# Kernel tuning notes

Measured on AMD Instinct MI355X. Metric: run time of the kernel, lower is better.

The kernel has to match this reference:

```python
import jax, jax.numpy as jnp
import numpy as np

B, S, D, H = 64, 512, 256, 512  # batch, seq_len, input embed dim, LSTM hidden dim


def setup_inputs() -> dict:
    key = jax.random.key(0)
    k1, k2, k3, k4, k5 = jax.random.split(key, 5)
    scale = 1.0 / np.sqrt(H)
    return {
        "state_embeds": jax.random.normal(k1, (B, S, D), dtype=jnp.float32),
        "W_ih": jax.random.normal(k2, (4 * H, D), dtype=jnp.float32) * scale,
        "W_hh": jax.random.normal(k3, (4 * H, H), dtype=jnp.float32) * scale,
        "b_ih": jax.random.normal(k4, (4 * H,), dtype=jnp.float32) * scale,
        "b_hh": jax.random.normal(k5, (4 * H,), dtype=jnp.float32) * scale,
        "h0": jnp.zeros((B, H), dtype=jnp.float32),
        "c0": jnp.zeros((B, H), dtype=jnp.float32),
    }


def reference(state_embeds, W_ih, W_hh, b_ih, b_hh, h0, c0):
    # Precompute the input projection for all timesteps at once: [B, S, 4H]
    x_proj = jnp.einsum("bsd,gd->bsg", state_embeds, W_ih) + b_ih + b_hh

    def step(carry, xt):
        h, c = carry
        gates = xt + h @ W_hh.T  # [B, 4H]
        i, f, g, o = jnp.split(gates, 4, axis=-1)
        i = jax.nn.sigmoid(i)
        f = jax.nn.sigmoid(f)
        g = jnp.tanh(g)
        o = jax.nn.sigmoid(o)
        c_new = f * c + i * g
        h_new = o * jnp.tanh(c_new)
        return (h_new, c_new), h_new

    (hT, cT), hs = jax.lax.scan(step, (h0, c0), jnp.swapaxes(x_proj, 0, 1))
    embeddings = jnp.swapaxes(hs, 0, 1)  # [B, S, H]
    # hidden state is detached in the original; here we just return it
    return embeddings, hT, cT
```

## Files before the change

kernel.cpp:

```cpp
#include <hip/hip_runtime.h>
#include <hip/hip_bf16.h>


#define NB 64
#define NS 512
#define ND 256
#define NH 512
#define FLAG_MAGIC 0x41000000
#define PLANE_ELEMS (NB * NH)

typedef __bf16 bf16x8 __attribute__((ext_vector_type(8)));
typedef float  f32x4  __attribute__((ext_vector_type(4)));

union Frag {
  bf16x8 v;
  unsigned long long u[2];
  __bf16 e[8];
};

__device__ __forceinline__ float bf2f(__bf16 b) {
  unsigned short us = __builtin_bit_cast(unsigned short, b);
  unsigned int ui = ((unsigned int)us) << 16;
  return __builtin_bit_cast(float, ui);
}

__device__ __forceinline__ void hilo8(const float* vals, Frag& fh, Frag& fl) {
#pragma unroll
  for (int j = 0; j < 8; ++j) {
    __bf16 hi = (__bf16)vals[j];
    float r = vals[j] - bf2f(hi);
    fh.e[j] = hi;
    fl.e[j] = (__bf16)r;
  }
}

__device__ __forceinline__ float fsigmoid(float x) {
  return 1.0f / (1.0f + __expf(-x));
}
__device__ __forceinline__ float ftanh(float x) {
  float t = fminf(fmaxf(2.0f * x, -30.0f), 30.0f);
  float e = __expf(t);
  return (e - 1.0f) / (e + 1.0f);
}

__global__ __launch_bounds__(128, 1)
void lstm_xp(const float* __restrict__ x,
             const float* __restrict__ Wih,
             const float* __restrict__ Whh,
             const float* __restrict__ bih,
             const float* __restrict__ bhh,
             const float* __restrict__ h0,
             const float* __restrict__ c0,
             float* __restrict__ out,
             int* __restrict__ flags,
             unsigned short* __restrict__ hring,
             unsigned short* __restrict__ lring,
             float4* __restrict__ xproj)
{
  const int tid  = threadIdx.x;
  const int lane = tid & 63;
  const int wv   = tid >> 6;
  const int team = blockIdx.x >> 6;
  const int wg   = blockIdx.x & 63;
  const int l15  = lane & 15;
  const int quad = lane >> 4;
  const int hb   = wg * 8 + wv * 4;
  const int myb  = team * 16 + l15;
  const int myh  = hb + quad;

  int* flagsT = flags + team * 64;
  if (tid == 0)
    __hip_atomic_store(flagsT + wg, FLAG_MAGIC, __ATOMIC_RELAXED,
                       __HIP_MEMORY_SCOPE_AGENT);

  const int jA = l15 >> 2;
  const int gA = l15 & 3;
  const int rA = gA * NH + hb + jA;
  bf16x8 Ahi[24], Alo[24];
  {
    const float* wi = Wih + rA * ND;
    const float* wh = Whh + rA * NH;
#pragma unroll
    for (int c = 0; c < 24; ++c) {
      int k0 = c * 32 + quad * 8;
      const float* src = (c < 8) ? (wi + k0) : (wh + (k0 - 256));
      float4 f0 = *(const float4*)(src);
      float4 f1 = *(const float4*)(src + 4);
      float vals[8] = {f0.x, f0.y, f0.z, f0.w, f1.x, f1.y, f1.z, f1.w};
      Frag fh, fl;
      hilo8(vals, fh, fl);
      Ahi[c] = fh.v;
      Alo[c] = fl.v;
    }
  }

  float bias[4];
#pragma unroll
  for (int g = 0; g < 4; ++g)
    bias[g] = bih[g * NH + myh] + bhh[g * NH + myh];

  float4* xpw = xproj + ((size_t)(blockIdx.x * 2 + wv)) * NS * 64;
#pragma unroll 1
  for (int t = 0; t < NS; ++t) {
    float4 xf[16];
    const float* xr = x + (myb * NS + t) * ND + quad * 8;
#pragma unroll
    for (int c = 0; c < 8; ++c) {
      xf[2 * c]     = *(const float4*)(xr + 32 * c);
      xf[2 * c + 1] = *(const float4*)(xr + 32 * c + 4);
    }
    f32x4 a_hh = {bias[0], bias[1], bias[2], bias[3]};
    f32x4 a_hl = {0.f, 0.f, 0.f, 0.f};
    f32x4 a_lh = {0.f, 0.f, 0.f, 0.f};
#pragma unroll
    for (int c = 0; c < 8; ++c) {
      float vals[8] = {xf[2*c].x, xf[2*c].y, xf[2*c].z, xf[2*c].w,
                       xf[2*c+1].x, xf[2*c+1].y, xf[2*c+1].z, xf[2*c+1].w};
      Frag bh, bl;
      hilo8(vals, bh, bl);
      a_hh = __builtin_amdgcn_mfma_f32_16x16x32_bf16(Ahi[c], bh.v, a_hh, 0, 0, 0);
      a_hl = __builtin_amdgcn_mfma_f32_16x16x32_bf16(Ahi[c], bl.v, a_hl, 0, 0, 0);
      a_lh = __builtin_amdgcn_mfma_f32_16x16x32_bf16(Alo[c], bh.v, a_lh, 0, 0, 0);
    }
    float4 xpv;
    xpv.x = a_hh[0] + a_hl[0] + a_lh[0];
    xpv.y = a_hh[1] + a_hl[1] + a_lh[1];
    xpv.z = a_hh[2] + a_hl[2] + a_lh[2];
    xpv.w = a_hh[3] + a_hl[3] + a_lh[3];
    xpw[t * 64 + lane] = xpv;
  }
  asm volatile("s_waitcnt vmcnt(0)" ::: "memory");

  float c_st  = c0[myb * NH + myh];
  float h_val = 0.0f;
  float4 xp_cur = xpw[lane];

#pragma unroll 1
  for (int t = 0; t < NS; ++t) {
    f32x4 a_hh = {0.f, 0.f, 0.f, 0.f};
    f32x4 a_hl = {0.f, 0.f, 0.f, 0.f};
    f32x4 a_lh = {0.f, 0.f, 0.f, 0.f};

    if (t > 0) {
      while (true) {
        int fl = __hip_atomic_load(flagsT + lane, __ATOMIC_RELAXED,
                                   __HIP_MEMORY_SCOPE_AGENT);
        unsigned int d = (unsigned int)(fl - FLAG_MAGIC);
        if (__all(d >= (unsigned int)t && d <= 512u)) break;
        __builtin_amdgcn_s_sleep(1);
      }
      asm volatile("" ::: "memory");

      const unsigned short* hbp = hring + (t - 1) * PLANE_ELEMS + myb * NH + quad * 8;
      const unsigned short* lbp = lring + (t - 1) * PLANE_ELEMS + myb * NH + quad * 8;
#pragma unroll
      for (int c = 8; c < 24; ++c) {
        int off = 32 * (c - 8);
        Frag bh, bl;
        bh.v = *(const bf16x8*)(hbp + off);
        bl.v = *(const bf16x8*)(lbp + off);
        a_hh = __builtin_amdgcn_mfma_f32_16x16x32_bf16(Ahi[c], bh.v, a_hh, 0, 0, 0);
        a_hl = __builtin_amdgcn_mfma_f32_16x16x32_bf16(Ahi[c], bl.v, a_hl, 0, 0, 0);
        a_lh = __builtin_amdgcn_mfma_f32_16x16x32_bf16(Alo[c], bh.v, a_lh, 0, 0, 0);
      }
    } else {
      const float* hr = h0 + myb * NH + quad * 8;
#pragma unroll
      for (int c = 8; c < 24; ++c) {
        int off = 32 * (c - 8);
        float4 f0 = *(const float4*)(hr + off);
        float4 f1 = *(const float4*)(hr + off + 4);
        float vals[8] = {f0.x, f0.y, f0.z, f0.w, f1.x, f1.y, f1.z, f1.w};
        Frag bh, bl;
        hilo8(vals, bh, bl);
        a_hh = __builtin_amdgcn_mfma_f32_16x16x32_bf16(Ahi[c], bh.v, a_hh, 0, 0, 0);
        a_hl = __builtin_amdgcn_mfma_f32_16x16x32_bf16(Ahi[c], bl.v, a_hl, 0, 0, 0);
        a_lh = __builtin_amdgcn_mfma_f32_16x16x32_bf16(Alo[c], bh.v, a_lh, 0, 0, 0);
      }
    }

    float pre_i = xp_cur.x + a_hh[0] + a_hl[0] + a_lh[0];
    float pre_f = xp_cur.y + a_hh[1] + a_hl[1] + a_lh[1];
    float pre_g = xp_cur.z + a_hh[2] + a_hl[2] + a_lh[2];
    float pre_o = xp_cur.w + a_hh[3] + a_hl[3] + a_lh[3];
    float gi = fsigmoid(pre_i);
    float gf = fsigmoid(pre_f);
    float gg = ftanh(pre_g);
    float go = fsigmoid(pre_o);
    c_st  = gf * c_st + gi * gg;
    h_val = go * ftanh(c_st);

    __bf16 hh = (__bf16)h_val;
    float  rr = h_val - bf2f(hh);
    __bf16 hl = (__bf16)rr;
    unsigned int uh = (unsigned int)__builtin_bit_cast(unsigned short, hh);
    unsigned int ul = (unsigned int)__builtin_bit_cast(unsigned short, hl);
    unsigned int ph = (unsigned int)__shfl_xor((int)uh, 16, 64);
    unsigned int pl = (unsigned int)__shfl_xor((int)ul, 16, 64);
    if ((quad & 1) == 0) {
      int eoff = t * PLANE_ELEMS + myb * NH + myh;
      __hip_atomic_store((unsigned int*)(hring + eoff), uh | (ph << 16),
                         __ATOMIC_RELAXED, __HIP_MEMORY_SCOPE_AGENT);
      __hip_atomic_store((unsigned int*)(lring + eoff), ul | (pl << 16),
                         __ATOMIC_RELAXED, __HIP_MEMORY_SCOPE_AGENT);
    }

    asm volatile("s_waitcnt vmcnt(0)" ::: "memory");
    __syncthreads();
    if (tid == 0)
      __hip_atomic_store(flagsT + wg, FLAG_MAGIC + t + 1, __ATOMIC_RELAXED,
                         __HIP_MEMORY_SCOPE_AGENT);

    out[(myb * NS + t) * NH + myh] = h_val;
    if (t + 1 < NS) xp_cur = xpw[(t + 1) * 64 + lane];
  }

  const int obase = NB * NS * NH;
  out[obase + myb * NH + myh] = h_val;
  out[obase + NB * NH + myb * NH + myh] = c_st;
}

__global__ __launch_bounds__(128, 1)
void lstm_ring(const float* __restrict__ x,
               const float* __restrict__ Wih,
               const float* __restrict__ Whh,
               const float* __restrict__ bih,
               const float* __restrict__ bhh,
               const float* __restrict__ h0,
               const float* __restrict__ c0,
               float* __restrict__ out,
               int* __restrict__ flags,
               unsigned short* __restrict__ hring,
               unsigned short* __restrict__ lring)
{
  const int tid  = threadIdx.x;
  const int lane = tid & 63;
  const int wv   = tid >> 6;
  const int team = blockIdx.x >> 6;
  const int wg   = blockIdx.x & 63;
  const int l15  = lane & 15;
  const int quad = lane >> 4;
  const int hb   = wg * 8 + wv * 4;
  const int myb  = team * 16 + l15;
  const int myh  = hb + quad;

  int* flagsT = flags + team * 64;
  if (tid == 0)
    __hip_atomic_store(flagsT + wg, FLAG_MAGIC, __ATOMIC_RELAXED,
                       __HIP_MEMORY_SCOPE_AGENT);

  const int jA = l15 >> 2;
  const int gA = l15 & 3;
  const int rA = gA * NH + hb + jA;
  bf16x8 Ahi[24], Alo[24];
  {
    const float* wi = Wih + rA * ND;
    const float* wh = Whh + rA * NH;
#pragma unroll
    for (int c = 0; c < 24; ++c) {
      int k0 = c * 32 + quad * 8;
      const float* src = (c < 8) ? (wi + k0) : (wh + (k0 - 256));
      float4 f0 = *(const float4*)(src);
      float4 f1 = *(const float4*)(src + 4);
      float vals[8] = {f0.x, f0.y, f0.z, f0.w, f1.x, f1.y, f1.z, f1.w};
      Frag fh, fl;
      hilo8(vals, fh, fl);
      Ahi[c] = fh.v;
      Alo[c] = fl.v;
    }
  }

  float bias[4];
#pragma unroll
  for (int g = 0; g < 4; ++g)
    bias[g] = bih[g * NH + myh] + bhh[g * NH + myh];

  float c_st  = c0[myb * NH + myh];
  float h_val = 0.0f;

#pragma unroll 1
  for (int t = 0; t < NS; ++t) {
    float4 xf[16];
    const float* xr = x + (myb * NS + t) * ND + quad * 8;
#pragma unroll
    for (int c = 0; c < 8; ++c) {
      xf[2 * c]     = *(const float4*)(xr + 32 * c);
      xf[2 * c + 1] = *(const float4*)(xr + 32 * c + 4);
    }

    f32x4 a_hh = {bias[0], bias[1], bias[2], bias[3]};
    f32x4 a_hl = {0.f, 0.f, 0.f, 0.f};
    f32x4 a_lh = {0.f, 0.f, 0.f, 0.f};

#pragma unroll
    for (int c = 0; c < 8; ++c) {
      float vals[8] = {xf[2*c].x, xf[2*c].y, xf[2*c].z, xf[2*c].w,
                       xf[2*c+1].x, xf[2*c+1].y, xf[2*c+1].z, xf[2*c+1].w};
      Frag bh, bl;
      hilo8(vals, bh, bl);
      a_hh = __builtin_amdgcn_mfma_f32_16x16x32_bf16(Ahi[c], bh.v, a_hh, 0, 0, 0);
      a_hl = __builtin_amdgcn_mfma_f32_16x16x32_bf16(Ahi[c], bl.v, a_hl, 0, 0, 0);
      a_lh = __builtin_amdgcn_mfma_f32_16x16x32_bf16(Alo[c], bh.v, a_lh, 0, 0, 0);
    }

    if (t > 0) {
      while (true) {
        int fl = __hip_atomic_load(flagsT + lane, __ATOMIC_RELAXED,
                                   __HIP_MEMORY_SCOPE_AGENT);
        unsigned int d = (unsigned int)(fl - FLAG_MAGIC);
        if (__all(d >= (unsigned int)t && d <= 512u)) break;
        __builtin_amdgcn_s_sleep(1);
      }
      asm volatile("" ::: "memory");

      const unsigned short* hbp = hring + (t - 1) * PLANE_ELEMS + myb * NH + quad * 8;
      const unsigned short* lbp = lring + (t - 1) * PLANE_ELEMS + myb * NH + quad * 8;
#pragma unroll
      for (int c = 8; c < 24; ++c) {
        int off = 32 * (c - 8);
        Frag bh, bl;
        bh.v = *(const bf16x8*)(hbp + off);
        bl.v = *(const bf16x8*)(lbp + off);
        a_hh = __builtin_amdgcn_mfma_f32_16x16x32_bf16(Ahi[c], bh.v, a_hh, 0, 0, 0);
        a_hl = __builtin_amdgcn_mfma_f32_16x16x32_bf16(Ahi[c], bl.v, a_hl, 0, 0, 0);
        a_lh = __builtin_amdgcn_mfma_f32_16x16x32_bf16(Alo[c], bh.v, a_lh, 0, 0, 0);
      }
    } else {
      const float* hr = h0 + myb * NH + quad * 8;
#pragma unroll
      for (int c = 8; c < 24; ++c) {
        int off = 32 * (c - 8);
        float4 f0 = *(const float4*)(hr + off);
        float4 f1 = *(const float4*)(hr + off + 4);
        float vals[8] = {f0.x, f0.y, f0.z, f0.w, f1.x, f1.y, f1.z, f1.w};
        Frag bh, bl;
        hilo8(vals, bh, bl);
        a_hh = __builtin_amdgcn_mfma_f32_16x16x32_bf16(Ahi[c], bh.v, a_hh, 0, 0, 0);
        a_hl = __builtin_amdgcn_mfma_f32_16x16x32_bf16(Ahi[c], bl.v, a_hl, 0, 0, 0);
        a_lh = __builtin_amdgcn_mfma_f32_16x16x32_bf16(Alo[c], bh.v, a_lh, 0, 0, 0);
      }
    }

    float pre_i = a_hh[0] + a_hl[0] + a_lh[0];
    float pre_f = a_hh[1] + a_hl[1] + a_lh[1];
    float pre_g = a_hh[2] + a_hl[2] + a_lh[2];
    float pre_o = a_hh[3] + a_hl[3] + a_lh[3];
    float gi = fsigmoid(pre_i);
    float gf = fsigmoid(pre_f);
    float gg = ftanh(pre_g);
    float go = fsigmoid(pre_o);
    c_st  = gf * c_st + gi * gg;
    h_val = go * ftanh(c_st);

    __bf16 hh = (__bf16)h_val;
    float  rr = h_val - bf2f(hh);
    __bf16 hl = (__bf16)rr;
    unsigned int uh = (unsigned int)__builtin_bit_cast(unsigned short, hh);
    unsigned int ul = (unsigned int)__builtin_bit_cast(unsigned short, hl);
    unsigned int ph = (unsigned int)__shfl_xor((int)uh, 16, 64);
    unsigned int pl = (unsigned int)__shfl_xor((int)ul, 16, 64);
    if ((quad & 1) == 0) {
      int eoff = t * PLANE_ELEMS + myb * NH + myh;
      __hip_atomic_store((unsigned int*)(hring + eoff), uh | (ph << 16),
                         __ATOMIC_RELAXED, __HIP_MEMORY_SCOPE_AGENT);
      __hip_atomic_store((unsigned int*)(lring + eoff), ul | (pl << 16),
                         __ATOMIC_RELAXED, __HIP_MEMORY_SCOPE_AGENT);
    }

    asm volatile("s_waitcnt vmcnt(0)" ::: "memory");
    __syncthreads();
    if (tid == 0)
      __hip_atomic_store(flagsT + wg, FLAG_MAGIC + t + 1, __ATOMIC_RELAXED,
                         __HIP_MEMORY_SCOPE_AGENT);

    out[(myb * NS + t) * NH + myh] = h_val;
  }

  const int obase = NB * NS * NH;
  out[obase + myb * NH + myh] = h_val;
  out[obase + NB * NH + myb * NH + myh] = c_st;
}

extern "C" void kernel_launch(void* const* d_in, const int* in_sizes, int n_in,
                              void* d_out, int out_size, void* d_ws, size_t ws_size,
                              hipStream_t stream) {
  const float* x   = (const float*)d_in[0];
  const float* Wih = (const float*)d_in[1];
  const float* Whh = (const float*)d_in[2];
  const float* bih = (const float*)d_in[3];
  const float* bhh = (const float*)d_in[4];
  const float* h0  = (const float*)d_in[5];
  const float* c0  = (const float*)d_in[6];
  float* out = (float*)d_out;

  char* ws = (char*)d_ws;
  int* flags = (int*)ws;

  const size_t ringBytes  = (size_t)NS * PLANE_ELEMS * sizeof(unsigned short);
  const size_t xprojBytes = (size_t)512 * NS * 64 * sizeof(float4);
  const size_t need_ring  = 4096 + 2 * ringBytes;
  const size_t need_full  = need_ring + xprojBytes;

  unsigned short* hring = (unsigned short*)(ws + 4096);
  unsigned short* lring = (unsigned short*)(ws + 4096 + ringBytes);

  if (ws_size >= need_full) {
    float4* xproj = (float4*)(ws + need_ring);
    lstm_xp<<<dim3(256), dim3(128), 0, stream>>>(
        x, Wih, Whh, bih, bhh, h0, c0, out, flags, hring, lring, xproj);
  } else {
    lstm_ring<<<dim3(256), dim3(128), 0, stream>>>(
        x, Wih, Whh, bih, bhh, h0, c0, out, flags, hring, lring);
  }
}
```

Before: 4.421 ms.

## Pin each LSTM team to one XCC and sync through local L2

Launches 512 blocks and has half of them exit immediately. Team is chosen as blockIdx&7, so under round-robin dispatch each 64-block team lands on a single XCC. Blocks record their XCC ID and wait on a global ready counter; if a team's mask shows exactly one XCC, the team uses workgroup-scope ring and flag stores and sc0 polling, which stay in that XCC's L2. A slow agent-scope backup flag is read occasionally, and an agent-scope path remains for mixed placement. It also drops the separate x-projection precompute pass and its workspace buffer, folding the input projection back into each timestep. The goal is to cut cross-XCC coherence latency on the per-step barrier, at the cost of relying on dispatch placement and on all 256 working blocks being co-resident.

New measurement: 4.791 ms. +8.4%, slower.

```diff
diff --git a/kernel.cpp b/kernel.cpp
--- a/kernel.cpp
+++ b/kernel.cpp
@@ -1,5 +1,4 @@
 #include <hip/hip_runtime.h>
-#include <hip/hip_bf16.h>
 
 
 #define NB 64
@@ -8,6 +7,7 @@
 #define NH 512
 #define FLAG_MAGIC 0x41000000
 #define PLANE_ELEMS (NB * NH)
+#define NWORK 256
 
 typedef __bf16 bf16x8 __attribute__((ext_vector_type(8)));
 typedef float  f32x4  __attribute__((ext_vector_type(4)));
@@ -43,8 +43,154 @@
   return (e - 1.0f) / (e + 1.0f);
 }
 
+__device__ __forceinline__ int poll_sc0(const int* p) {
+  int v;
+  asm volatile("global_load_dword %0, %1, off sc0\n\ts_waitcnt vmcnt(0)"
+               : "=&v"(v) : "v"(p) : "memory");
+  return v;
+}
+
+template<bool FAST>
+__device__ __forceinline__ void run_lstm(
+    const float* __restrict__ x, const float* __restrict__ h0,
+    const float* __restrict__ c0, float* __restrict__ out,
+    int* flagsT, int* flagsBT,
+    unsigned short* __restrict__ hring, unsigned short* __restrict__ lring,
+    const bf16x8* Ahi, const bf16x8* Alo, const float* bias,
+    int tid, int lane, int wg, int quad, int myb, int myh)
+{
+  float c_st  = c0[myb * NH + myh];
+  float h_val = 0.0f;
+
+#pragma unroll 1
+  for (int t = 0; t < NS; ++t) {
+    float4 xf[16];
+    const float* xr = x + (myb * NS + t) * ND + quad * 8;
+#pragma unroll
+    for (int c = 0; c < 8; ++c) {
+      xf[2 * c]     = *(const float4*)(xr + 32 * c);
+      xf[2 * c + 1] = *(const float4*)(xr + 32 * c + 4);
+    }
+    f32x4 a_hh = {bias[0], bias[1], bias[2], bias[3]};
+    f32x4 a_hl = {0.f, 0.f, 0.f, 0.f};
+    f32x4 a_lh = {0.f, 0.f, 0.f, 0.f};
+#pragma unroll
+    for (int c = 0; c < 8; ++c) {
+      float vals[8] = {xf[2*c].x, xf[2*c].y, xf[2*c].z, xf[2*c].w,
+                       xf[2*c+1].x, xf[2*c+1].y, xf[2*c+1].z, xf[2*c+1].w};
+      Frag bh, bl;
+      hilo8(vals, bh, bl);
+      a_hh = __builtin_amdgcn_mfma_f32_16x16x32_bf16(Ahi[c], bh.v, a_hh, 0, 0, 0);
+      a_hl = __builtin_amdgcn_mfma_f32_16x16x32_bf16(Ahi[c], bl.v, a_hl, 0, 0, 0);
+      a_lh = __builtin_amdgcn_mfma_f32_16x16x32_bf16(Alo[c], bh.v, a_lh, 0, 0, 0);
+    }
+
+    if (t > 0) {
+      int spin = 0;
+      while (true) {
+        int fl;
+        if (FAST) {
+          fl = poll_sc0(flagsT + lane);
+          if ((++spin & 8191) == 0) {
+            int fb = __hip_atomic_load(flagsBT + lane, __ATOMIC_RELAXED,
+                                       __HIP_MEMORY_SCOPE_AGENT);
+            if (fb > fl) fl = fb;
+          }
+        } else {
+          fl = __hip_atomic_load(flagsT + lane, __ATOMIC_RELAXED,
+                                 __HIP_MEMORY_SCOPE_AGENT);
+        }
+        unsigned int d = (unsigned int)(fl - FLAG_MAGIC);
+        if (__all(d >= (unsigned int)t && d <= 512u)) break;
+        __builtin_amdgcn_s_sleep(1);
+      }
+      asm volatile("" ::: "memory");
+
+      const unsigned short* hbp = hring + (t - 1) * PLANE_ELEMS + myb * NH + quad * 8;
+      const unsigned short* lbp = lring + (t - 1) * PLANE_ELEMS + myb * NH + quad * 8;
+#pragma unroll
+      for (int c = 8; c < 24; ++c) {
+        int off = 32 * (c - 8);
+        Frag bh, bl;
+        bh.v = *(const bf16x8*)(hbp + off);
+        bl.v = *(const bf16x8*)(lbp + off);
+        a_hh = __builtin_amdgcn_mfma_f32_16x16x32_bf16(Ahi[c], bh.v, a_hh, 0, 0, 0);
+        a_hl = __builtin_amdgcn_mfma_f32_16x16x32_bf16(Ahi[c], bl.v, a_hl, 0, 0, 0);
+        a_lh = __builtin_amdgcn_mfma_f32_16x16x32_bf16(Alo[c], bh.v, a_lh, 0, 0, 0);
+      }
+    } else {
+      const float* hr = h0 + myb * NH + quad * 8;
+#pragma unroll
+      for (int c = 8; c < 24; ++c) {
+        int off = 32 * (c - 8);
+        float4 f0 = *(const float4*)(hr + off);
+        float4 f1 = *(const float4*)(hr + off + 4);
+        float vals[8] = {f0.x, f0.y, f0.z, f0.w, f1.x, f1.y, f1.z, f1.w};
+        Frag bh, bl;
+        hilo8(vals, bh, bl);
+        a_hh = __builtin_amdgcn_mfma_f32_16x16x32_bf16(Ahi[c], bh.v, a_hh, 0, 0, 0);
+        a_hl = __builtin_amdgcn_mfma_f32_16x16x32_bf16(Ahi[c], bl.v, a_hl, 0, 0, 0);
+        a_lh = __builtin_amdgcn_mfma_f32_16x16x32_bf16(Alo[c], bh.v, a_lh, 0, 0, 0);
+      }
+    }
+
+    float pre_i = a_hh[0] + a_hl[0] + a_lh[0];
+    float pre_f = a_hh[1] + a_hl[1] + a_lh[1];
+    float pre_g = a_hh[2] + a_hl[2] + a_lh[2];
+    float pre_o = a_hh[3] + a_hl[3] + a_lh[3];
+    float gi = fsigmoid(pre_i);
+    float gf = fsigmoid(pre_f);
+    float gg = ftanh(pre_g);
+    float go = fsigmoid(pre_o);
+    c_st  = gf * c_st + gi * gg;
+    h_val = go * ftanh(c_st);
+
+    __bf16 hh = (__bf16)h_val;
+    float  rr = h_val - bf2f(hh);
+    __bf16 hl = (__bf16)rr;
+    unsigned int uh = (unsigned int)__builtin_bit_cast(unsigned short, hh);
+    unsigned int ul = (unsigned int)__builtin_bit_cast(unsigned short, hl);
+    unsigned int ph = (unsigned int)__shfl_xor((int)uh, 16, 64);
+    unsigned int pl = (unsigned int)__shfl_xor((int)ul, 16, 64);
+    if ((quad & 1) == 0) {
+      int eoff = t * PLANE_ELEMS + myb * NH + myh;
+      if (FAST) {
+        __hip_atomic_store((unsigned int*)(hring + eoff), uh | (ph << 16),
+                           __ATOMIC_RELAXED, __HIP_MEMORY_SCOPE_WORKGROUP);
+        __hip_atomic_store((unsigned int*)(lring + eoff), ul | (pl << 16),
+                           __ATOMIC_RELAXED, __HIP_MEMORY_SCOPE_WORKGROUP);
+      } else {
+        __hip_atomic_store((unsigned int*)(hring + eoff), uh | (ph << 16),
+                           __ATOMIC_RELAXED, __HIP_MEMORY_SCOPE_AGENT);
+        __hip_atomic_store((unsigned int*)(lring + eoff), ul | (pl << 16),
+                           __ATOMIC_RELAXED, __HIP_MEMORY_SCOPE_AGENT);
+      }
+    }
+
+    asm volatile("s_waitcnt vmcnt(0)" ::: "memory");
+    __syncthreads();
+    if (tid == 0) {
+      if (FAST) {
+        __hip_atomic_store(flagsT + wg, FLAG_MAGIC + t + 1,
+                           __ATOMIC_RELAXED, __HIP_MEMORY_SCOPE_WORKGROUP);
+        __hip_atomic_store(flagsBT + wg, FLAG_MAGIC + t + 1,
+                           __ATOMIC_RELAXED, __HIP_MEMORY_SCOPE_AGENT);
+      } else {
+        __hip_atomic_store(flagsT + wg, FLAG_MAGIC + t + 1,
+                           __ATOMIC_RELAXED, __HIP_MEMORY_SCOPE_AGENT);
+      }
+    }
+
+    out[(myb * NS + t) * NH + myh] = h_val;
+  }
+
+  const int obase = NB * NS * NH;
+  out[obase + myb * NH + myh] = h_val;
+  out[obase + NB * NH + myb * NH + myh] = c_st;
+}
+
 __global__ __launch_bounds__(128, 1)
-void lstm_xp(const float* __restrict__ x,
+void lstm_l2(const float* __restrict__ x,
              const float* __restrict__ Wih,
              const float* __restrict__ Whh,
              const float* __restrict__ bih,
@@ -52,26 +198,33 @@
              const float* __restrict__ h0,
              const float* __restrict__ c0,
              float* __restrict__ out,
-             int* __restrict__ flags,
+             int* flags, int* flagsB, int* ready, unsigned int* masks,
              unsigned short* __restrict__ hring,
-             unsigned short* __restrict__ lring,
-             float4* __restrict__ xproj)
+             unsigned short* __restrict__ lring)
 {
+  const int b = blockIdx.x;
+  if ((b & 7) >= 4) return;
+  const int team = b & 7;
+  const int wg   = b >> 3;
   const int tid  = threadIdx.x;
   const int lane = tid & 63;
   const int wv   = tid >> 6;
-  const int team = blockIdx.x >> 6;
-  const int wg   = blockIdx.x & 63;
   const int l15  = lane & 15;
   const int quad = lane >> 4;
   const int hb   = wg * 8 + wv * 4;
   const int myb  = team * 16 + l15;
   const int myh  = hb + quad;
 
-  int* flagsT = flags + team * 64;
-  if (tid == 0)
-    __hip_atomic_store(flagsT + wg, FLAG_MAGIC, __ATOMIC_RELAXED,
-                       __HIP_MEMORY_SCOPE_AGENT);
+  int* flagsT  = flags  + team * 64;
+  int* flagsBT = flagsB + team * 64;
+
+  int xcc;
+  asm volatile("s_getreg_b32 %0, hwreg(HW_REG_XCC_ID)" : "=s"(xcc));
+  if (tid == 0) {
+    __hip_atomic_fetch_or(&masks[team], 1u << (xcc & 31),
+                          __ATOMIC_RELAXED, __HIP_MEMORY_SCOPE_AGENT);
+    __hip_atomic_fetch_add(ready, 1, __ATOMIC_RELEASE, __HIP_MEMORY_SCOPE_AGENT);
+  }
 
   const int jA = l15 >> 2;
   const int gA = l15 & 3;
@@ -99,286 +252,23 @@
   for (int g = 0; g < 4; ++g)
     bias[g] = bih[g * NH + myh] + bhh[g * NH + myh];
 
-  float4* xpw = xproj + ((size_t)(blockIdx.x * 2 + wv)) * NS * 64;
-#pragma unroll 1
-  for (int t = 0; t < NS; ++t) {
-    float4 xf[16];
-    const float* xr = x + (myb * NS + t) * ND + quad * 8;
-#pragma unroll
-    for (int c = 0; c < 8; ++c) {
-      xf[2 * c]     = *(const float4*)(xr + 32 * c);
-      xf[2 * c + 1] = *(const float4*)(xr + 32 * c + 4);
-    }
-    f32x4 a_hh = {bias[0], bias[1], bias[2], bias[3]};
-    f32x4 a_hl = {0.f, 0.f, 0.f, 0.f};
-    f32x4 a_lh = {0.f, 0.f, 0.f, 0.f};
-#pragma unroll
-    for (int c = 0; c < 8; ++c) {
-      float vals[8] = {xf[2*c].x, xf[2*c].y, xf[2*c].z, xf[2*c].w,
-                       xf[2*c+1].x, xf[2*c+1].y, xf[2*c+1].z, xf[2*c+1].w};
-      Frag bh, bl;
-      hilo8(vals, bh, bl);
-      a_hh = __builtin_amdgcn_mfma_f32_16x16x32_bf16(Ahi[c], bh.v, a_hh, 0, 0, 0);
-      a_hl = __builtin_amdgcn_mfma_f32_16x16x32_bf16(Ahi[c], bl.v, a_hl, 0, 0, 0);
-      a_lh = __builtin_amdgcn_mfma_f32_16x16x32_bf16(Alo[c], bh.v, a_lh, 0, 0, 0);
-    }
-    float4 xpv;
-    xpv.x = a_hh[0] + a_hl[0] + a_lh[0];
-    xpv.y = a_hh[1] + a_hl[1] + a_lh[1];
-    xpv.z = a_hh[2] + a_hl[2] + a_lh[2];
-    xpv.w = a_hh[3] + a_hl[3] + a_lh[3];
-    xpw[t * 64 + lane] = xpv;
-  }
-  asm volatile("s_waitcnt vmcnt(0)" ::: "memory");
-
-  float c_st  = c0[myb * NH + myh];
-  float h_val = 0.0f;
-  float4 xp_cur = xpw[lane];
-
-#pragma unroll 1
-  for (int t = 0; t < NS; ++t) {
-    f32x4 a_hh = {0.f, 0.f, 0.f, 0.f};
-    f32x4 a_hl = {0.f, 0.f, 0.f, 0.f};
-    f32x4 a_lh = {0.f, 0.f, 0.f, 0.f};
-
-    if (t > 0) {
-      while (true) {
-        int fl = __hip_atomic_load(flagsT + lane, __ATOMIC_RELAXED,
-                                   __HIP_MEMORY_SCOPE_AGENT);
-        unsigned int d = (unsigned int)(fl - FLAG_MAGIC);
-        if (__all(d >= (unsigned int)t && d <= 512u)) break;
-        __builtin_amdgcn_s_sleep(1);
-      }
-      asm volatile("" ::: "memory");
-
-      const unsigned short* hbp = hring + (t - 1) * PLANE_ELEMS + myb * NH + quad * 8;
-      const unsigned short* lbp = lring + (t - 1) * PLANE_ELEMS + myb * NH + quad * 8;
-#pragma unroll
-      for (int c = 8; c < 24; ++c) {
-        int off = 32 * (c - 8);
-        Frag bh, bl;
-        bh.v = *(const bf16x8*)(hbp + off);
-        bl.v = *(const bf16x8*)(lbp + off);
-        a_hh = __builtin_amdgcn_mfma_f32_16x16x32_bf16(Ahi[c], bh.v, a_hh, 0, 0, 0);
-        a_hl = __builtin_amdgcn_mfma_f32_16x16x32_bf16(Ahi[c], bl.v, a_hl, 0, 0, 0);
-        a_lh = __builtin_amdgcn_mfma_f32_16x16x32_bf16(Alo[c], bh.v, a_lh, 0, 0, 0);
-      }
-    } else {
-      const float* hr = h0 + myb * NH + quad * 8;
-#pragma unroll
-      for (int c = 8; c < 24; ++c) {
-        int off = 32 * (c - 8);
-        float4 f0 = *(const float4*)(hr + off);
-        float4 f1 = *(const float4*)(hr + off + 4);
-        float vals[8] = {f0.x, f0.y, f0.z, f0.w, f1.x, f1.y, f1.z, f1.w};
-        Frag bh, bl;
-        hilo8(vals, bh, bl);
-        a_hh = __builtin_amdgcn_mfma_f32_16x16x32_bf16(Ahi[c], bh.v, a_hh, 0, 0, 0);
-        a_hl = __builtin_amdgcn_mfma_f32_16x16x32_bf16(Ahi[c], bl.v, a_hl, 0, 0, 0);
-        a_lh = __builtin_amdgcn_mfma_f32_16x16x32_bf16(Alo[c], bh.v, a_lh, 0, 0, 0);
-      }
-    }
-
-    float pre_i = xp_cur.x + a_hh[0] + a_hl[0] + a_lh[0];
-    float pre_f = xp_cur.y + a_hh[1] + a_hl[1] + a_lh[1];
-    float pre_g = xp_cur.z + a_hh[2] + a_hl[2] + a_lh[2];
-    float pre_o = xp_cur.w + a_hh[3] + a_hl[3] + a_lh[3];
-    float gi = fsigmoid(pre_i);
-    float gf = fsigmoid(pre_f);
-    float gg = ftanh(pre_g);
-    float go = fsigmoid(pre_o);
-    c_st  = gf * c_st + gi * gg;
-    h_val = go * ftanh(c_st);
-
-    __bf16 hh = (__bf16)h_val;
-    float  rr = h_val - bf2f(hh);
-    __bf16 hl = (__bf16)rr;
-    unsigned int uh = (unsigned int)__builtin_bit_cast(unsigned short, hh);
-    unsigned int ul = (unsigned int)__builtin_bit_cast(unsigned short, hl);
-    unsigned int ph = (unsigned int)__shfl_xor((int)uh, 16, 64);
-    unsigned int pl = (unsigned int)__shfl_xor((int)ul, 16, 64);
-    if ((quad & 1) == 0) {
-      int eoff = t * PLANE_ELEMS + myb * NH + myh;
-      __hip_atomic_store((unsigned int*)(hring + eoff), uh | (ph << 16),
-                         __ATOMIC_RELAXED, __HIP_MEMORY_SCOPE_AGENT);
-      __hip_atomic_store((unsigned int*)(lring + eoff), ul | (pl << 16),
-                         __ATOMIC_RELAXED, __HIP_MEMORY_SCOPE_AGENT);
-    }
-
-    asm volatile("s_waitcnt vmcnt(0)" ::: "memory");
-    __syncthreads();
-    if (tid == 0)
-      __hip_atomic_store(flagsT + wg, FLAG_MAGIC + t + 1, __ATOMIC_RELAXED,
-                         __HIP_MEMORY_SCOPE_AGENT);
-
-    out[(myb * NS + t) * NH + myh] = h_val;
-    if (t + 1 < NS) xp_cur = xpw[(t + 1) * 64 + lane];
-  }
-
-  const int obase = NB * NS * NH;
-  out[obase + myb * NH + myh] = h_val;
-  out[obase + NB * NH + myb * NH + myh] = c_st;
-}
-
-__global__ __launch_bounds__(128, 1)
-void lstm_ring(const float* __restrict__ x,
-               const float* __restrict__ Wih,
-               const float* __restrict__ Whh,
-               const float* __restrict__ bih,
-               const float* __restrict__ bhh,
-               const float* __restrict__ h0,
-               const float* __restrict__ c0,
-               float* __restrict__ out,
-               int* __restrict__ flags,
-               unsigned short* __restrict__ hring,
-               unsigned short* __restrict__ lring)
-{
-  const int tid  = threadIdx.x;
-  const int lane = tid & 63;
-  const int wv   = tid >> 6;
-  const int team = blockIdx.x >> 6;
-  const int wg   = blockIdx.x & 63;
-  const int l15  = lane & 15;
-  const int quad = lane >> 4;
-  const int hb   = wg * 8 + wv * 4;
-  const int myb  = team * 16 + l15;
-  const int myh  = hb + quad;
-
-  int* flagsT = flags + team * 64;
-  if (tid == 0)
-    __hip_atomic_store(flagsT + wg, FLAG_MAGIC, __ATOMIC_RELAXED,
-                       __HIP_MEMORY_SCOPE_AGENT);
-
-  const int jA = l15 >> 2;
-  const int gA = l15 & 3;
-  const int rA = gA * NH + hb + jA;
-  bf16x8 Ahi[24], Alo[24];
-  {
-    const float* wi = Wih + rA * ND;
-    const float* wh = Whh + rA * NH;
-#pragma unroll
-    for (int c = 0; c < 24; ++c) {
-      int k0 = c * 32 + quad * 8;
-      const float* src = (c < 8) ? (wi + k0) : (wh + (k0 - 256));
-      float4 f0 = *(const float4*)(src);
-      float4 f1 = *(const float4*)(src + 4);
-      float vals[8] = {f0.x, f0.y, f0.z, f0.w, f1.x, f1.y, f1.z, f1.w};
-      Frag fh, fl;
-      hilo8(vals, fh, fl);
-      Ahi[c] = fh.v;
-      Alo[c] = fl.v;
-    }
-  }
-
-  float bias[4];
-#pragma unroll
-  for (int g = 0; g < 4; ++g)
-    bias[g] = bih[g * NH + myh] + bhh[g * NH + myh];
-
-  float c_st  = c0[myb * NH + myh];
-  float h_val = 0.0f;
-
-#pragma unroll 1
-  for (int t = 0; t < NS; ++t) {
-    float4 xf[16];
-    const float* xr = x + (myb * NS + t) * ND + quad * 8;
-#pragma unroll
-    for (int c = 0; c < 8; ++c) {
-      xf[2 * c]     = *(const float4*)(xr + 32 * c);
-      xf[2 * c + 1] = *(const float4*)(xr + 32 * c + 4);
-    }
-
-    f32x4 a_hh = {bias[0], bias[1], bias[2], bias[3]};
-    f32x4 a_hl = {0.f, 0.f, 0.f, 0.f};
-    f32x4 a_lh = {0.f, 0.f, 0.f, 0.f};
-
-#pragma unroll
-    for (int c = 0; c < 8; ++c) {
-      float vals[8] = {xf[2*c].x, xf[2*c].y, xf[2*c].z, xf[2*c].w,
-                       xf[2*c+1].x, xf[2*c+1].y, xf[2*c+1].z, xf[2*c+1].w};
-      Frag bh, bl;
-      hilo8(vals, bh, bl);
-      a_hh = __builtin_amdgcn_mfma_f32_16x16x32_bf16(Ahi[c], bh.v, a_hh, 0, 0, 0);
-      a_hl = __builtin_amdgcn_mfma_f32_16x16x32_bf16(Ahi[c], bl.v, a_hl, 0, 0, 0);
-      a_lh = __builtin_amdgcn_mfma_f32_16x16x32_bf16(Alo[c], bh.v, a_lh, 0, 0, 0);
-    }
-
-    if (t > 0) {
-      while (true) {
-        int fl = __hip_atomic_load(flagsT + lane, __ATOMIC_RELAXED,
-                                   __HIP_MEMORY_SCOPE_AGENT);
-        unsigned int d = (unsigned int)(fl - FLAG_MAGIC);
-        if (__all(d >= (unsigned int)t && d <= 512u)) break;
-        __builtin_amdgcn_s_sleep(1);
-      }
-      asm volatile("" ::: "memory");
-
-      const unsigned short* hbp = hring + (t - 1) * PLANE_ELEMS + myb * NH + quad * 8;
-      const unsigned short* lbp = lring + (t - 1) * PLANE_ELEMS + myb * NH + quad * 8;
-#pragma unroll
-      for (int c = 8; c < 24; ++c) {
-        int off = 32 * (c - 8);
-        Frag bh, bl;
-        bh.v = *(const bf16x8*)(hbp + off);
-        bl.v = *(const bf16x8*)(lbp + off);
-        a_hh = __builtin_amdgcn_mfma_f32_16x16x32_bf16(Ahi[c], bh.v, a_hh, 0, 0, 0);
-        a_hl = __builtin_amdgcn_mfma_f32_16x16x32_bf16(Ahi[c], bl.v, a_hl, 0, 0, 0);
-        a_lh = __builtin_amdgcn_mfma_f32_16x16x32_bf16(Alo[c], bh.v, a_lh, 0, 0, 0);
-      }
-    } else {
-      const float* hr = h0 + myb * NH + quad * 8;
-#pragma unroll
-      for (int c = 8; c < 24; ++c) {
-        int off = 32 * (c - 8);
-        float4 f0 = *(const float4*)(hr + off);
-        float4 f1 = *(const float4*)(hr + off + 4);
-        float vals[8] = {f0.x, f0.y, f0.z, f0.w, f1.x, f1.y, f1.z, f1.w};
-        Frag bh, bl;
-        hilo8(vals, bh, bl);
-        a_hh = __builtin_amdgcn_mfma_f32_16x16x32_bf16(Ahi[c], bh.v, a_hh, 0, 0, 0);
-        a_hl = __builtin_amdgcn_mfma_f32_16x16x32_bf16(Ahi[c], bl.v, a_hl, 0, 0, 0);
-        a_lh = __builtin_amdgcn_mfma_f32_16x16x32_bf16(Alo[c], bh.v, a_lh, 0, 0, 0);
-      }
-    }
-
-    float pre_i = a_hh[0] + a_hl[0] + a_lh[0];
-    float pre_f = a_hh[1] + a_hl[1] + a_lh[1];
-    float pre_g = a_hh[2] + a_hl[2] + a_lh[2];
-    float pre_o = a_hh[3] + a_hl[3] + a_lh[3];
-    float gi = fsigmoid(pre_i);
-    float gf = fsigmoid(pre_f);
-    float gg = ftanh(pre_g);
-    float go = fsigmoid(pre_o);
-    c_st  = gf * c_st + gi * gg;
-    h_val = go * ftanh(c_st);
-
-    __bf16 hh = (__bf16)h_val;
-    float  rr = h_val - bf2f(hh);
-    __bf16 hl = (__bf16)rr;
-    unsigned int uh = (unsigned int)__builtin_bit_cast(unsigned short, hh);
-    unsigned int ul = (unsigned int)__builtin_bit_cast(unsigned short, hl);
-    unsigned int ph = (unsigned int)__shfl_xor((int)uh, 16, 64);
-    unsigned int pl = (unsigned int)__shfl_xor((int)ul, 16, 64);
-    if ((quad & 1) == 0) {
-      int eoff = t * PLANE_ELEMS + myb * NH + myh;
-      __hip_atomic_store((unsigned int*)(hring + eoff), uh | (ph << 16),
-                         __ATOMIC_RELAXED, __HIP_MEMORY_SCOPE_AGENT);
-      __hip_atomic_store((unsigned int*)(lring + eoff), ul | (pl << 16),
-                         __ATOMIC_RELAXED, __HIP_MEMORY_SCOPE_AGENT);
-    }
-
-    asm volatile("s_waitcnt vmcnt(0)" ::: "memory");
-    __syncthreads();
-    if (tid == 0)
-      __hip_atomic_store(flagsT + wg, FLAG_MAGIC + t + 1, __ATOMIC_RELAXED,
-                         __HIP_MEMORY_SCOPE_AGENT);
-
-    out[(myb * NS + t) * NH + myh] = h_val;
-  }
-
-  const int obase = NB * NS * NH;
-  out[obase + myb * NH + myh] = h_val;
-  out[obase + NB * NH + myb * NH + myh] = c_st;
+  __shared__ int s_fast;
+  if (tid == 0) {
+    while (__hip_atomic_load(ready, __ATOMIC_ACQUIRE,
+                             __HIP_MEMORY_SCOPE_AGENT) < NWORK)
+      __builtin_amdgcn_s_sleep(2);
+    unsigned int m = __hip_atomic_load(&masks[team], __ATOMIC_RELAXED,
+                                       __HIP_MEMORY_SCOPE_AGENT);
+    s_fast = (__popc(m) == 1) ? 1 : 0;
+  }
+  __syncthreads();
+
+  if (s_fast)
+    run_lstm<true>(x, h0, c0, out, flagsT, flagsBT, hring, lring,
+                   Ahi, Alo, bias, tid, lane, wg, quad, myb, myh);
+  else
+    run_lstm<false>(x, h0, c0, out, flagsT, flagsBT, hring, lring,
+                    Ahi, Alo, bias, tid, lane, wg, quad, myb, myh);
 }
 
 extern "C" void kernel_launch(void* const* d_in, const int* in_sizes, int n_in,
@@ -394,22 +284,17 @@
   float* out = (float*)d_out;
 
   char* ws = (char*)d_ws;
-  int* flags = (int*)ws;
-
-  const size_t ringBytes  = (size_t)NS * PLANE_ELEMS * sizeof(unsigned short);
-  const size_t xprojBytes = (size_t)512 * NS * 64 * sizeof(float4);
-  const size_t need_ring  = 4096 + 2 * ringBytes;
-  const size_t need_full  = need_ring + xprojBytes;
-
+  int* flags  = (int*)ws;
+  int* ready  = (int*)(ws + 1024);
+  unsigned int* masks = (unsigned int*)(ws + 1028);
+  int* flagsB = (int*)(ws + 2048);
+  const size_t ringBytes = (size_t)NS * PLANE_ELEMS * sizeof(unsigned short);
   unsigned short* hring = (unsigned short*)(ws + 4096);
   unsigned short* lring = (unsigned short*)(ws + 4096 + ringBytes);
 
-  if (ws_size >= need_full) {
-    float4* xproj = (float4*)(ws + need_ring);
-    lstm_xp<<<dim3(256), dim3(128), 0, stream>>>(
-        x, Wih, Whh, bih, bhh, h0, c0, out, flags, hring, lring, xproj);
-  } else {
-    lstm_ring<<<dim3(256), dim3(128), 0, stream>>>(
-        x, Wih, Whh, bih, bhh, h0, c0, out, flags, hring, lring);
-  }
-}
+  hipMemsetAsync(ws, 0, 4096, stream);
+
+  lstm_l2<<<dim3(512), dim3(128), 0, stream>>>(
+      x, Wih, Whh, bih, bhh, h0, c0, out, flags, flagsB, ready, masks,
+      hring, lring);
+}
```
